# Performance work log

Measured on AMD Instinct MI355X. Metric: run time of the kernel, lower is better.

## Reference

```python
import jax, jax.numpy as jnp
import numpy as np

HQ = 32      # query heads
HKV = 8      # kv heads
DH = 128     # head dim
B, S, D = 8, 1, 4096
MAX_SEQ = 4096


def rope(x, pos):
    """Rotary embedding on interleaved pairs. x: [B,S,H,dh], pos: [S] int."""
    d = x.shape[-1]
    theta = 1.0 / (10000.0 ** (jnp.arange(0, d, 2, dtype=jnp.float32) / d))  # [d/2]
    ang = pos[:, None].astype(jnp.float32) * theta[None, :]                  # [S,d/2]
    cos = jnp.cos(ang)[None, :, None, :]
    sin = jnp.sin(ang)[None, :, None, :]
    xr, xi = x[..., 0::2], x[..., 1::2]
    out_r = xr * cos - xi * sin
    out_i = xr * sin + xi * cos
    return jnp.stack([out_r, out_i], axis=-1).reshape(x.shape)


def setup_inputs() -> dict:
    key = jax.random.key(0)
    ks = jax.random.split(key, 8)
    s = 0.02
    return {
        "x": jax.random.normal(ks[0], (B, S, D), jnp.float32),
        "wq": jax.random.normal(ks[1], (D, HQ * DH), jnp.float32) * s,
        "bq": jnp.zeros((HQ * DH,), jnp.float32),
        "wk": jax.random.normal(ks[2], (D, HKV * DH), jnp.float32) * s,
        "bk": jnp.zeros((HKV * DH,), jnp.float32),
        "wv": jax.random.normal(ks[3], (D, HKV * DH), jnp.float32) * s,
        "bv": jnp.zeros((HKV * DH,), jnp.float32),
        "wo": jax.random.normal(ks[4], (HQ * DH, D), jnp.float32) * s,
        "bo": jnp.zeros((D,), jnp.float32),
        "cache_k": jax.random.normal(ks[5], (B, MAX_SEQ, HKV, DH), jnp.float32) * 0.5,
        "cache_v": jax.random.normal(ks[6], (B, MAX_SEQ, HKV, DH), jnp.float32) * 0.5,
        "start_pos": MAX_SEQ - S,  # decode step at end of cache
    }


def reference(x, wq, bq, wk, bk, wv, bv, wo, bo, cache_k, cache_v, start_pos):
    b, s, d = x.shape
    n_rep = HQ // HKV
    q = (x @ wq + bq).reshape(b, s, HQ, DH)
    k = (x @ wk + bk).reshape(b, s, HKV, DH)
    v = (x @ wv + bv).reshape(b, s, HKV, DH)
    pos = start_pos + jnp.arange(s)
    q = rope(q, pos)
    k = rope(k, pos)
    # KV-cache scatter write
    cache_k = jax.lax.dynamic_update_slice(cache_k, k, (0, start_pos, 0, 0))
    cache_v = jax.lax.dynamic_update_slice(cache_v, v, (0, start_pos, 0, 0))
    t = start_pos + s  # static (start_pos is a Python int)
    keys = cache_k[:, :t]    # [B,T,HKV,DH]
    values = cache_v[:, :t]
    # repeat_kv: duplicate each kv head n_rep times -> [B,T,HQ,DH]
    keys = jnp.repeat(keys, n_rep, axis=2)
    values = jnp.repeat(values, n_rep, axis=2)
    # naive softmax attention, score matrix materialized
    scores = jnp.einsum("bshd,bthd->bhst", q, keys) * (DH ** -0.5)  # [B,HQ,S,T]
    attn = jax.nn.softmax(scores, axis=-1)
    out = jnp.einsum("bhst,bthd->bshd", attn, values).reshape(b, s, HQ * DH)
    return out @ wo + bo
```

## Files before the change

### kernel.cpp

```cpp
#include <hip/hip_runtime.h>
#include <cmath>

#define NB 8
#define DIM 4096
#define NHQ 32
#define NHKV 8
#define NDH 128
#define MAXSEQ 4096
#define STARTPOS 4095
#define QKV_COLS 6144
#define RCHUNK 64
#define NRC 64
#define SCALE 0.08838834764831845f
#define NCHUNK 64
#define CPOS 64

#define DOT4(k, qq) ((k).x*(qq).x + (k).y*(qq).y + (k).z*(qq).z + (k).w*(qq).w)

__global__ __launch_bounds__(256) void qkv_partial_k(
    const float* __restrict__ x, const float* __restrict__ wq,
    const float* __restrict__ wk, const float* __restrict__ wv,
    float* __restrict__ part) {
  int bid = blockIdx.x;
  int ct = bid % 12, rc = bid / 12;
  int tid = threadIdx.x;
  const float* W; int ldw; int colbase;
  int gcolbase = ct * 512;
  if (ct < 8)       { W = wq; ldw = NHQ * NDH;  colbase = gcolbase; }
  else if (ct < 10) { W = wk; ldw = NHKV * NDH; colbase = gcolbase - 4096; }
  else              { W = wv; ldw = NHKV * NDH; colbase = gcolbase - 5120; }

  __shared__ __align__(16) float xs[RCHUNK][8];
  int rbase = rc * RCHUNK;
  for (int i = tid; i < RCHUNK * 8; i += 256) {
    int b = i >> 6, r = i & 63;
    xs[r][b] = x[b * DIM + rbase + r];
  }
  __syncthreads();

  int col = colbase + tid * 2;
  const float* wp = W + (size_t)rbase * ldw + col;
  float2 acc[8];
#pragma unroll
  for (int b = 0; b < 8; b++) { acc[b].x = 0.f; acc[b].y = 0.f; }

#pragma unroll 8
  for (int r = 0; r < RCHUNK; r++) {
    float2 w2 = *(const float2*)wp; wp += ldw;
    float4 xa = *(const float4*)&xs[r][0];
    float4 xb = *(const float4*)&xs[r][4];
    acc[0].x += xa.x * w2.x; acc[0].y += xa.x * w2.y;
    acc[1].x += xa.y * w2.x; acc[1].y += xa.y * w2.y;
    acc[2].x += xa.z * w2.x; acc[2].y += xa.z * w2.y;
    acc[3].x += xa.w * w2.x; acc[3].y += xa.w * w2.y;
    acc[4].x += xb.x * w2.x; acc[4].y += xb.x * w2.y;
    acc[5].x += xb.y * w2.x; acc[5].y += xb.y * w2.y;
    acc[6].x += xb.z * w2.x; acc[6].y += xb.z * w2.y;
    acc[7].x += xb.w * w2.x; acc[7].y += xb.w * w2.y;
  }
  int gcol = gcolbase + tid * 2;
#pragma unroll
  for (int b = 0; b < 8; b++)
    *(float2*)&part[((size_t)rc * 8 + b) * QKV_COLS + gcol] = acc[b];
}

__global__ __launch_bounds__(256) void qkv_reduce_rope_k(
    const float* __restrict__ part, const float* __restrict__ bq,
    const float* __restrict__ bk, const float* __restrict__ bv,
    float* __restrict__ qws, float* __restrict__ kws, float* __restrict__ vws) {
  int idx = blockIdx.x * 256 + threadIdx.x;
  int b = idx / QKV_COLS, col = idx % QKV_COLS;
  float s = 0.f;
#pragma unroll 8
  for (int rcc = 0; rcc < NRC; rcc++)
    s += part[((size_t)rcc * 8 + b) * QKV_COLS + col];
  float bias = (col < 4096) ? bq[col] : (col < 5120 ? bk[col - 4096] : bv[col - 5120]);
  s += bias;
  float outv = s;
  if (col < 5120) {
    int dim = col & 127;
    int i2 = dim & ~1;
    float theta = powf(10000.f, -(float)i2 * (1.f / 128.f));
    float ang = (float)STARTPOS * theta;
    float c = cosf(ang), sn = sinf(ang);
    float other = __shfl_xor(s, 1);
    if ((col & 1) == 0) outv = s * c - other * sn;
    else                outv = other * sn + s * c;
  }
  if (col < 4096)       qws[b * 4096 + col] = outv;
  else if (col < 5120)  kws[b * 1024 + (col - 4096)] = outv;
  else                  vws[b * 1024 + (col - 5120)] = outv;
}

__global__ __launch_bounds__(256, 2) void attn_chunk_k(
    const float* __restrict__ qws, const float* __restrict__ kws,
    const float* __restrict__ vws, const float* __restrict__ ck,
    const float* __restrict__ cv, float* __restrict__ pm,
    float* __restrict__ pl, float* __restrict__ pacc) {
  int bid = blockIdx.x;
  int chunk = bid & 63, b = bid >> 6;
  int tid = threadIdx.x;
  int w = tid >> 6, lane = tid & 63;
  int half = lane >> 5, s32 = lane & 31;
  int hkv = w * 2 + half;
  int t0 = chunk * CPOS;

  __shared__ float sbuf[NHKV][4][65];
  __shared__ float marr[NHQ];

  const float* qb = qws + ((size_t)b * NHQ + hkv * 4) * NDH + s32 * 4;
  float4 qf0 = *(const float4*)(qb + 0 * NDH);
  float4 qf1 = *(const float4*)(qb + 1 * NDH);
  float4 qf2 = *(const float4*)(qb + 2 * NDH);
  float4 qf3 = *(const float4*)(qb + 3 * NDH);

  const float* kbase = ck + ((size_t)(b * MAXSEQ + t0) * NHKV + hkv) * NDH + s32 * 4;
  const float* vbase = cv + ((size_t)(b * MAXSEQ + t0) * NHKV + hkv) * NDH + s32 * 4;
  const float* kwsrow = kws + ((size_t)b * NHKV + hkv) * NDH + s32 * 4;
  const float* vwsrow = vws + ((size_t)b * NHKV + hkv) * NDH + s32 * 4;

  for (int ii = 0; ii < CPOS; ii += 8) {
    float4 kf[8];
#pragma unroll
    for (int u = 0; u < 8; u++) {
      int t = t0 + ii + u;
      const float* kr = (t == STARTPOS) ? kwsrow : (kbase + (size_t)(ii + u) * 1024);
      kf[u] = *(const float4*)kr;
    }
#pragma unroll
    for (int u = 0; u < 8; u++) {
      float p0 = DOT4(kf[u], qf0);
      float p1 = DOT4(kf[u], qf1);
      float p2 = DOT4(kf[u], qf2);
      float p3 = DOT4(kf[u], qf3);
      p0 += __shfl_xor(p0, 1); p0 += __shfl_xor(p0, 2);
      p1 += __shfl_xor(p1, 1); p1 += __shfl_xor(p1, 2);
      p2 += __shfl_xor(p2, 1); p2 += __shfl_xor(p2, 2);
      p3 += __shfl_xor(p3, 1); p3 += __shfl_xor(p3, 2);
      int hsel = s32 & 3;
      float v = (hsel == 0) ? p0 : (hsel == 1) ? p1 : (hsel == 2) ? p2 : p3;
      v += __shfl_xor(v, 4); v += __shfl_xor(v, 8); v += __shfl_xor(v, 16);
      v *= SCALE;
      if (s32 < 4) sbuf[hkv][s32][ii + u] = v;
    }
  }
  __syncthreads();

  {
    int hq = tid >> 3, sub = tid & 7;
    int hk = hq >> 2, hh = hq & 3;
    float m = -1e30f;
#pragma unroll
    for (int k = 0; k < 8; k++) m = fmaxf(m, sbuf[hk][hh][sub + k * 8]);
    m = fmaxf(m, __shfl_xor(m, 1));
    m = fmaxf(m, __shfl_xor(m, 2));
    m = fmaxf(m, __shfl_xor(m, 4));
    float l = 0.f;
#pragma unroll
    for (int k = 0; k < 8; k++) l += expf(sbuf[hk][hh][sub + k * 8] - m);
    l += __shfl_xor(l, 1);
    l += __shfl_xor(l, 2);
    l += __shfl_xor(l, 4);
    if (sub == 0) {
      pm[(size_t)bid * NHQ + hq] = m;
      pl[(size_t)bid * NHQ + hq] = l;
      marr[hq] = m;
    }
  }
  __syncthreads();
  {
    int hq = tid >> 3, sub = tid & 7;
    int hk = hq >> 2, hh = hq & 3;
    float m = marr[hq];
#pragma unroll
    for (int k = 0; k < 8; k++) {
      int t = sub + k * 8;
      sbuf[hk][hh][t] = expf(sbuf[hk][hh][t] - m);
    }
  }
  __syncthreads();

  float4 acc0 = {0.f, 0.f, 0.f, 0.f};
  float4 acc1 = {0.f, 0.f, 0.f, 0.f};
  float4 acc2 = {0.f, 0.f, 0.f, 0.f};
  float4 acc3 = {0.f, 0.f, 0.f, 0.f};
  for (int ii = 0; ii < CPOS; ii += 8) {
    float4 vf[8];
#pragma unroll
    for (int u = 0; u < 8; u++) {
      int t = t0 + ii + u;
      const float* vr = (t == STARTPOS) ? vwsrow : (vbase + (size_t)(ii + u) * 1024);
      vf[u] = *(const float4*)vr;
    }
#pragma unroll
    for (int u = 0; u < 8; u++) {
      int tl = ii + u;
      float pp0 = sbuf[hkv][0][tl];
      float pp1 = sbuf[hkv][1][tl];
      float pp2 = sbuf[hkv][2][tl];
      float pp3 = sbuf[hkv][3][tl];
      acc0.x += pp0 * vf[u].x; acc0.y += pp0 * vf[u].y;
      acc0.z += pp0 * vf[u].z; acc0.w += pp0 * vf[u].w;
      acc1.x += pp1 * vf[u].x; acc1.y += pp1 * vf[u].y;
      acc1.z += pp1 * vf[u].z; acc1.w += pp1 * vf[u].w;
      acc2.x += pp2 * vf[u].x; acc2.y += pp2 * vf[u].y;
      acc2.z += pp2 * vf[u].z; acc2.w += pp2 * vf[u].w;
      acc3.x += pp3 * vf[u].x; acc3.y += pp3 * vf[u].y;
      acc3.z += pp3 * vf[u].z; acc3.w += pp3 * vf[u].w;
    }
  }

  float* pb = pacc + ((size_t)bid * NHQ + hkv * 4) * NDH + s32 * 4;
  *(float4*)(pb + 0 * NDH) = acc0;
  *(float4*)(pb + 1 * NDH) = acc1;
  *(float4*)(pb + 2 * NDH) = acc2;
  *(float4*)(pb + 3 * NDH) = acc3;
}

__global__ __launch_bounds__(128) void attn_combine_k(
    const float* __restrict__ pm, const float* __restrict__ pl,
    const float* __restrict__ pacc, float* __restrict__ aout) {
  int bid = blockIdx.x;
  int b = bid >> 5, hq = bid & 31;
  int d = threadIdx.x;
  float M = -1e30f;
  for (int c = 0; c < NCHUNK; c++)
    M = fmaxf(M, pm[((size_t)(b * NCHUNK + c)) * NHQ + hq]);
  float L = 0.f, o = 0.f;
  for (int c = 0; c < NCHUNK; c++) {
    size_t idx = (size_t)(b * NCHUNK + c) * NHQ + hq;
    float wgt = expf(pm[idx] - M);
    L += wgt * pl[idx];
    o += wgt * pacc[idx * NDH + d];
  }
  aout[(size_t)b * 4096 + hq * NDH + d] = o / L;
}

__global__ __launch_bounds__(256) void out_partial_k(
    const float* __restrict__ ain, const float* __restrict__ wo,
    float* __restrict__ part) {
  int bid = blockIdx.x;
  int ct = bid & 7, rc = bid >> 3;
  int tid = threadIdx.x;
  __shared__ __align__(16) float xs[RCHUNK][8];
  int rbase = rc * RCHUNK;
  for (int i = tid; i < RCHUNK * 8; i += 256) {
    int b = i >> 6, r = i & 63;
    xs[r][b] = ain[(size_t)b * 4096 + rbase + r];
  }
  __syncthreads();

  int col = ct * 512 + tid * 2;
  const float* wp = wo + (size_t)rbase * 4096 + col;
  float2 acc[8];
#pragma unroll
  for (int b = 0; b < 8; b++) { acc[b].x = 0.f; acc[b].y = 0.f; }
#pragma unroll 8
  for (int r = 0; r < RCHUNK; r++) {
    float2 w2 = *(const float2*)wp; wp += 4096;
    float4 xa = *(const float4*)&xs[r][0];
    float4 xb = *(const float4*)&xs[r][4];
    acc[0].x += xa.x * w2.x; acc[0].y += xa.x * w2.y;
    acc[1].x += xa.y * w2.x; acc[1].y += xa.y * w2.y;
    acc[2].x += xa.z * w2.x; acc[2].y += xa.z * w2.y;
    acc[3].x += xa.w * w2.x; acc[3].y += xa.w * w2.y;
    acc[4].x += xb.x * w2.x; acc[4].y += xb.x * w2.y;
    acc[5].x += xb.y * w2.x; acc[5].y += xb.y * w2.y;
    acc[6].x += xb.z * w2.x; acc[6].y += xb.z * w2.y;
    acc[7].x += xb.w * w2.x; acc[7].y += xb.w * w2.y;
  }
#pragma unroll
  for (int b = 0; b < 8; b++)
    *(float2*)&part[((size_t)rc * 8 + b) * 4096 + col] = acc[b];
}

__global__ __launch_bounds__(256) void out_reduce_k(
    const float* __restrict__ part, const float* __restrict__ bo,
    float* __restrict__ out) {
  int idx = blockIdx.x * 256 + threadIdx.x;
  int b = idx >> 12, col = idx & 4095;
  float s = bo[col];
#pragma unroll 8
  for (int rcc = 0; rcc < NRC; rcc++)
    s += part[((size_t)rcc * 8 + b) * 4096 + col];
  out[idx] = s;
  (void)b;
}

extern "C" void kernel_launch(void* const* d_in, const int* in_sizes, int n_in,
                              void* d_out, int out_size, void* d_ws, size_t ws_size,
                              hipStream_t stream) {
  const float* x       = (const float*)d_in[0];
  const float* wq      = (const float*)d_in[1];
  const float* bq      = (const float*)d_in[2];
  const float* wk      = (const float*)d_in[3];
  const float* bk      = (const float*)d_in[4];
  const float* wv      = (const float*)d_in[5];
  const float* bv      = (const float*)d_in[6];
  const float* wo      = (const float*)d_in[7];
  const float* bo      = (const float*)d_in[8];
  const float* cache_k = (const float*)d_in[9];
  const float* cache_v = (const float*)d_in[10];
  float* out = (float*)d_out;

  float* ws = (float*)d_ws;
  float* qkv_part = ws;
  float* pacc     = ws;
  float* wo_part  = ws;
  float* qws  = ws + 3145728;
  float* kws  = ws + 3178496;
  float* vws  = ws + 3186688;
  float* pm   = ws + 3194880;
  float* pl   = ws + 3211264;
  float* aout = ws + 3227648;

  qkv_partial_k<<<768, 256, 0, stream>>>(x, wq, wk, wv, qkv_part);
  qkv_reduce_rope_k<<<192, 256, 0, stream>>>(qkv_part, bq, bk, bv, qws, kws, vws);
  attn_chunk_k<<<512, 256, 0, stream>>>(qws, kws, vws, cache_k, cache_v, pm, pl, pacc);
  attn_combine_k<<<256, 128, 0, stream>>>(pm, pl, pacc, aout);
  out_partial_k<<<512, 256, 0, stream>>>(aout, wo, wo_part);
  out_reduce_k<<<128, 256, 0, stream>>>(wo_part, bo, out);
}
```

Measured before the change: 125.1 us.

## Split attention chunk positions across warp pairs with 512-thread blocks

The attention chunk kernel now uses 512 threads, with each pair of waves splitting the 64 cache positions by parity so each wave handles half the loads. This raises memory-level parallelism for the KV cache read. The new-token K/V substitution is moved out of the inner loops into a chunk-63 fix-up: a separate score computation and a V-delta correction. The softmax passes are merged into one, and partial accumulators are reduced through shared memory. Costs are an extra sync, shared-memory traffic, and more register pressure from the unrolled score buffer.

```diff
diff --git a/kernel.cpp b/kernel.cpp
--- a/kernel.cpp
+++ b/kernel.cpp
@@ -92,7 +92,7 @@
   else                  vws[b * 1024 + (col - 5120)] = outv;
 }
 
-__global__ __launch_bounds__(256, 2) void attn_chunk_k(
+__global__ __launch_bounds__(512, 4) void attn_pair_k(
     const float* __restrict__ qws, const float* __restrict__ kws,
     const float* __restrict__ vws, const float* __restrict__ ck,
     const float* __restrict__ cv, float* __restrict__ pm,
@@ -102,11 +102,12 @@
   int tid = threadIdx.x;
   int w = tid >> 6, lane = tid & 63;
   int half = lane >> 5, s32 = lane & 31;
-  int hkv = w * 2 + half;
+  int pairid = w >> 1, parity = w & 1;
+  int hkv = pairid * 2 + half;
   int t0 = chunk * CPOS;
 
-  __shared__ float sbuf[NHKV][4][65];
-  __shared__ float marr[NHQ];
+  __shared__ float sbuf[NHKV][4][CPOS + 1];
+  __shared__ __align__(16) float axl[4][64][20];
 
   const float* qb = qws + ((size_t)b * NHQ + hkv * 4) * NDH + s32 * 4;
   float4 qf0 = *(const float4*)(qb + 0 * NDH);
@@ -116,17 +117,14 @@
 
   const float* kbase = ck + ((size_t)(b * MAXSEQ + t0) * NHKV + hkv) * NDH + s32 * 4;
   const float* vbase = cv + ((size_t)(b * MAXSEQ + t0) * NHKV + hkv) * NDH + s32 * 4;
-  const float* kwsrow = kws + ((size_t)b * NHKV + hkv) * NDH + s32 * 4;
-  const float* vwsrow = vws + ((size_t)b * NHKV + hkv) * NDH + s32 * 4;
-
-  for (int ii = 0; ii < CPOS; ii += 8) {
+
+  float s_t[32];
+#pragma unroll
+  for (int ii = 0; ii < 32; ii += 8) {
     float4 kf[8];
 #pragma unroll
-    for (int u = 0; u < 8; u++) {
-      int t = t0 + ii + u;
-      const float* kr = (t == STARTPOS) ? kwsrow : (kbase + (size_t)(ii + u) * 1024);
-      kf[u] = *(const float4*)kr;
-    }
+    for (int u = 0; u < 8; u++)
+      kf[u] = *(const float4*)(kbase + (size_t)(2 * (ii + u) + parity) * 1024);
 #pragma unroll
     for (int u = 0; u < 8; u++) {
       float p0 = DOT4(kf[u], qf0);
@@ -138,45 +136,54 @@
       p2 += __shfl_xor(p2, 1); p2 += __shfl_xor(p2, 2);
       p3 += __shfl_xor(p3, 1); p3 += __shfl_xor(p3, 2);
       int hsel = s32 & 3;
-      float v = (hsel == 0) ? p0 : (hsel == 1) ? p1 : (hsel == 2) ? p2 : p3;
-      v += __shfl_xor(v, 4); v += __shfl_xor(v, 8); v += __shfl_xor(v, 16);
-      v *= SCALE;
-      if (s32 < 4) sbuf[hkv][s32][ii + u] = v;
+      s_t[ii + u] = (hsel == 0) ? p0 : (hsel == 1) ? p1 : (hsel == 2) ? p2 : p3;
     }
   }
+#pragma unroll
+  for (int j = 0; j < 32; j++) {
+    float v = s_t[j];
+    v += __shfl_xor(v, 4); v += __shfl_xor(v, 8); v += __shfl_xor(v, 16);
+    if (s32 < 4) sbuf[hkv][s32][2 * j + parity] = v * SCALE;
+  }
+  __syncthreads();
+
+  if (chunk == 63 && tid < NHQ) {
+    int hq = tid, hk = hq >> 2;
+    const float4* qp = (const float4*)(qws + ((size_t)b * NHQ + hq) * NDH);
+    const float4* kp = (const float4*)(kws + ((size_t)b * NHKV + hk) * NDH);
+    float s = 0.f;
+#pragma unroll
+    for (int j = 0; j < 32; j++) { float4 a = qp[j], c = kp[j]; s += DOT4(a, c); }
+    sbuf[hk][hq & 3][63] = s * SCALE;
+  }
   __syncthreads();
 
   {
-    int hq = tid >> 3, sub = tid & 7;
+    int hq = tid >> 4, sub = tid & 15;
     int hk = hq >> 2, hh = hq & 3;
-    float m = -1e30f;
-#pragma unroll
-    for (int k = 0; k < 8; k++) m = fmaxf(m, sbuf[hk][hh][sub + k * 8]);
+    float e0 = sbuf[hk][hh][sub];
+    float e1 = sbuf[hk][hh][sub + 16];
+    float e2 = sbuf[hk][hh][sub + 32];
+    float e3 = sbuf[hk][hh][sub + 48];
+    float m = fmaxf(fmaxf(e0, e1), fmaxf(e2, e3));
     m = fmaxf(m, __shfl_xor(m, 1));
     m = fmaxf(m, __shfl_xor(m, 2));
     m = fmaxf(m, __shfl_xor(m, 4));
-    float l = 0.f;
-#pragma unroll
-    for (int k = 0; k < 8; k++) l += expf(sbuf[hk][hh][sub + k * 8] - m);
+    m = fmaxf(m, __shfl_xor(m, 8));
+    float q0 = expf(e0 - m), q1 = expf(e1 - m), q2 = expf(e2 - m), q3 = expf(e3 - m);
+    float l = q0 + q1 + q2 + q3;
     l += __shfl_xor(l, 1);
     l += __shfl_xor(l, 2);
     l += __shfl_xor(l, 4);
+    l += __shfl_xor(l, 8);
     if (sub == 0) {
       pm[(size_t)bid * NHQ + hq] = m;
       pl[(size_t)bid * NHQ + hq] = l;
-      marr[hq] = m;
     }
-  }
-  __syncthreads();
-  {
-    int hq = tid >> 3, sub = tid & 7;
-    int hk = hq >> 2, hh = hq & 3;
-    float m = marr[hq];
-#pragma unroll
-    for (int k = 0; k < 8; k++) {
-      int t = sub + k * 8;
-      sbuf[hk][hh][t] = expf(sbuf[hk][hh][t] - m);
-    }
+    sbuf[hk][hh][sub] = q0;
+    sbuf[hk][hh][sub + 16] = q1;
+    sbuf[hk][hh][sub + 32] = q2;
+    sbuf[hk][hh][sub + 48] = q3;
   }
   __syncthreads();
 
@@ -184,17 +191,15 @@
   float4 acc1 = {0.f, 0.f, 0.f, 0.f};
   float4 acc2 = {0.f, 0.f, 0.f, 0.f};
   float4 acc3 = {0.f, 0.f, 0.f, 0.f};
-  for (int ii = 0; ii < CPOS; ii += 8) {
+#pragma unroll
+  for (int ii = 0; ii < 32; ii += 8) {
     float4 vf[8];
 #pragma unroll
+    for (int u = 0; u < 8; u++)
+      vf[u] = *(const float4*)(vbase + (size_t)(2 * (ii + u) + parity) * 1024);
+#pragma unroll
     for (int u = 0; u < 8; u++) {
-      int t = t0 + ii + u;
-      const float* vr = (t == STARTPOS) ? vwsrow : (vbase + (size_t)(ii + u) * 1024);
-      vf[u] = *(const float4*)vr;
-    }
-#pragma unroll
-    for (int u = 0; u < 8; u++) {
-      int tl = ii + u;
+      int tl = 2 * (ii + u) + parity;
       float pp0 = sbuf[hkv][0][tl];
       float pp1 = sbuf[hkv][1][tl];
       float pp2 = sbuf[hkv][2][tl];
@@ -209,12 +214,43 @@
       acc3.z += pp3 * vf[u].z; acc3.w += pp3 * vf[u].w;
     }
   }
-
-  float* pb = pacc + ((size_t)bid * NHQ + hkv * 4) * NDH + s32 * 4;
-  *(float4*)(pb + 0 * NDH) = acc0;
-  *(float4*)(pb + 1 * NDH) = acc1;
-  *(float4*)(pb + 2 * NDH) = acc2;
-  *(float4*)(pb + 3 * NDH) = acc3;
+  if (chunk == 63 && parity == 1) {
+    float4 vold = *(const float4*)(vbase + (size_t)63 * 1024);
+    float4 vnew = *(const float4*)(vws + ((size_t)b * NHKV + hkv) * NDH + s32 * 4);
+    float d0 = vnew.x - vold.x, d1 = vnew.y - vold.y,
+          d2 = vnew.z - vold.z, d3 = vnew.w - vold.w;
+    float pp0 = sbuf[hkv][0][63], pp1 = sbuf[hkv][1][63],
+          pp2 = sbuf[hkv][2][63], pp3 = sbuf[hkv][3][63];
+    acc0.x += pp0 * d0; acc0.y += pp0 * d1; acc0.z += pp0 * d2; acc0.w += pp0 * d3;
+    acc1.x += pp1 * d0; acc1.y += pp1 * d1; acc1.z += pp1 * d2; acc1.w += pp1 * d3;
+    acc2.x += pp2 * d0; acc2.y += pp2 * d1; acc2.z += pp2 * d2; acc2.w += pp2 * d3;
+    acc3.x += pp3 * d0; acc3.y += pp3 * d1; acc3.z += pp3 * d2; acc3.w += pp3 * d3;
+  }
+
+  if (parity == 1) {
+    float* dst = &axl[pairid][lane][0];
+    *(float4*)(dst + 0)  = acc0;
+    *(float4*)(dst + 4)  = acc1;
+    *(float4*)(dst + 8)  = acc2;
+    *(float4*)(dst + 12) = acc3;
+  }
+  __syncthreads();
+  if (parity == 0) {
+    const float* src = &axl[pairid][lane][0];
+    float4 b0 = *(const float4*)(src + 0);
+    float4 b1 = *(const float4*)(src + 4);
+    float4 b2 = *(const float4*)(src + 8);
+    float4 b3 = *(const float4*)(src + 12);
+    acc0.x += b0.x; acc0.y += b0.y; acc0.z += b0.z; acc0.w += b0.w;
+    acc1.x += b1.x; acc1.y += b1.y; acc1.z += b1.z; acc1.w += b1.w;
+    acc2.x += b2.x; acc2.y += b2.y; acc2.z += b2.z; acc2.w += b2.w;
+    acc3.x += b3.x; acc3.y += b3.y; acc3.z += b3.z; acc3.w += b3.w;
+    float* pb = pacc + ((size_t)bid * NHQ + hkv * 4) * NDH + s32 * 4;
+    *(float4*)(pb + 0 * NDH) = acc0;
+    *(float4*)(pb + 1 * NDH) = acc1;
+    *(float4*)(pb + 2 * NDH) = acc2;
+    *(float4*)(pb + 3 * NDH) = acc3;
+  }
 }
 
 __global__ __launch_bounds__(128) void attn_combine_k(
@@ -316,7 +352,7 @@
 
   qkv_partial_k<<<768, 256, 0, stream>>>(x, wq, wk, wv, qkv_part);
   qkv_reduce_rope_k<<<192, 256, 0, stream>>>(qkv_part, bq, bk, bv, qws, kws, vws);
-  attn_chunk_k<<<512, 256, 0, stream>>>(qws, kws, vws, cache_k, cache_v, pm, pl, pacc);
+  attn_pair_k<<<512, 512, 0, stream>>>(qws, kws, vws, cache_k, cache_v, pm, pl, pacc);
   attn_combine_k<<<256, 128, 0, stream>>>(pm, pl, pacc, aout);
   out_partial_k<<<512, 256, 0, stream>>>(aout, wo, wo_part);
   out_reduce_k<<<128, 256, 0, stream>>>(wo_part, bo, out);
```

New measurement: 133.3 us. 1.07x slower.
